# Performance work log

Hardware: AMD Instinct MI355X
Metric: run time of the kernel (lower is better)

Reference implementation:

```python
import jax, jax.numpy as jnp
import numpy as np

N_QUBITS = 4
N_LAYERS = 2
PROJ_DIM = 64
B = 262144
C64 = jnp.complex64


def setup_inputs() -> dict:
    key = jax.random.key(0)
    ks = jax.random.split(key, 4)
    x = jax.random.normal(ks[0], (B, N_QUBITS), dtype=jnp.float32)
    # TorchLayer default init: uniform(0, 2*pi)
    weights = jax.random.uniform(ks[1], (N_LAYERS, N_QUBITS, 3), dtype=jnp.float32) * (2.0 * np.pi)
    W = jax.random.normal(ks[2], (PROJ_DIM, N_QUBITS), dtype=jnp.float32) * 0.5
    b = jnp.zeros((PROJ_DIM,), dtype=jnp.float32)
    gamma = jnp.ones((PROJ_DIM,), dtype=jnp.float32)
    beta = jnp.zeros((PROJ_DIM,), dtype=jnp.float32)
    return {"x": x, "weights": weights, "W": W, "b": b, "gamma": gamma, "beta": beta}


def _apply_1q(state, U, w):
    # state: (B, 2,2,2,2); U: (2,2) shared or (B,2,2) per-sample
    s = jnp.moveaxis(state, 1 + w, -1)
    if U.ndim == 3:
        s = jnp.einsum('b...j,bij->b...i', s, U)
    else:
        s = s @ U.T
    return jnp.moveaxis(s, -1, 1 + w)


def _apply_cnot(state, c, t):
    s = jnp.moveaxis(state, (1 + c, 1 + t), (-2, -1))
    s = jnp.concatenate([s[..., :1, :], s[..., 1:, ::-1]], axis=-2)
    return jnp.moveaxis(s, (-2, -1), (1 + c, 1 + t))


def _rot_matrix(phi, theta, omega):
    # PennyLane Rot = RZ(omega) @ RY(theta) @ RZ(phi)
    c = jnp.cos(theta / 2).astype(C64)
    s = jnp.sin(theta / 2).astype(C64)
    ep = jnp.exp(-0.5j * (phi + omega).astype(C64))
    em = jnp.exp(0.5j * (phi - omega).astype(C64))
    return jnp.array(0, C64) + jnp.stack([
        jnp.stack([ep * c, -em * s]),
        jnp.stack([jnp.conj(em) * s, jnp.conj(ep) * c])], axis=0)


def _circuit(angles, weights):
    # angles: (B, n) real; returns (B, n) PauliZ expvals
    n = N_QUBITS
    Bn = angles.shape[0]
    state = jnp.zeros((Bn, 2 ** n), dtype=C64).at[:, 0].set(1.0)
    state = state.reshape((Bn,) + (2,) * n)
    # AngleEmbedding: RX(angle_w) on wire w (per-sample angles)
    half = angles / 2
    cos_h = jnp.cos(half).astype(C64)
    isin_h = (-1j) * jnp.sin(half).astype(C64)
    for w in range(n):
        U = jnp.stack([jnp.stack([cos_h[:, w], isin_h[:, w]], -1),
                       jnp.stack([isin_h[:, w], cos_h[:, w]], -1)], -2)  # (B,2,2)
        state = _apply_1q(state, U, w)
    # StronglyEntanglingLayers: Rot on each wire, then CNOT ring with range r
    for l in range(N_LAYERS):
        for w in range(n):
            U = _rot_matrix(weights[l, w, 0], weights[l, w, 1], weights[l, w, 2])
            state = _apply_1q(state, U, w)
        r = l % (n - 1) + 1
        for w in range(n):
            state = _apply_cnot(state, w, (w + r) % n)
    probs = jnp.abs(state) ** 2  # (B,2,...,2)
    sign = jnp.array([1.0, -1.0], dtype=jnp.float32)
    zs = []
    for w in range(n):
        axes = tuple(a for a in range(1, n + 1) if a != 1 + w)
        zs.append(probs.sum(axis=axes) @ sign)
    return jnp.stack(zs, -1)  # (B, n)


def reference(x, weights, W, b, gamma, beta):
    angles = jnp.tanh(x) * np.pi
    q = _circuit(angles, weights)            # (B, n_qubits)
    q = jax.nn.softmax(q, axis=-1)
    h = q @ W.T + b                          # (B, proj_dim)
    mu = h.mean(axis=-1, keepdims=True)
    var = ((h - mu) ** 2).mean(axis=-1, keepdims=True)
    hn = (h - mu) * jax.lax.rsqrt(var + 1e-5)
    return hn * gamma + beta
```

## Files before the change

### kernel.cpp

```cpp
#include <hip/hip_runtime.h>
#include <cstdint>


#define WS_VRT 0
#define WS_VIT 256
#define WS_A   512
#define WS_B0  768
#define WS_G   832
#define WS_g   848
#define WS_C0  852

__global__ __launch_bounds__(64) void qb_setup(const float* __restrict__ wts,
                                               const float* __restrict__ W,
                                               const float* __restrict__ bias,
                                               const float* __restrict__ gamma,
                                               float* __restrict__ ws) {
    const int lane = threadIdx.x;
    const int row  = lane >> 2;
    const int cg   = lane & 3;

    float ur[4], ui[4];
    #pragma unroll
    for (int c = 0; c < 4; ++c) {
        ur[c] = (row == 4*cg + c) ? 1.f : 0.f;
        ui[c] = 0.f;
    }

    #pragma unroll
    for (int l = 0; l < 2; ++l) {
        #pragma unroll
        for (int w = 0; w < 4; ++w) {
            const float ph = wts[l*12 + w*3 + 0];
            const float th = wts[l*12 + w*3 + 1];
            const float om = wts[l*12 + w*3 + 2];
            float st, ct; __sincosf(0.5f*th, &st, &ct);
            float sp, cp; __sincosf(0.5f*(ph+om), &sp, &cp);
            float sm, cm; __sincosf(0.5f*(ph-om), &sm, &cm);
            const float a00r =  cp*ct, a00i = -sp*ct;
            const float a01r = -cm*st, a01i = -sm*st;
            const float a10r =  cm*st, a10i = -sm*st;
            const float a11r =  cp*ct, a11i =  sp*ct;
            const int m8 = 8 >> w;
            const int xm = m8 << 2;
            const bool hi = (row & m8) != 0;
            #pragma unroll
            for (int c = 0; c < 4; ++c) {
                const float pr = __shfl_xor(ur[c], xm, 64);
                const float pi = __shfl_xor(ui[c], xm, 64);
                float nr, ni;
                if (!hi) {
                    nr = a00r*ur[c] - a00i*ui[c] + a01r*pr - a01i*pi;
                    ni = a00r*ui[c] + a00i*ur[c] + a01r*pi + a01i*pr;
                } else {
                    nr = a11r*ur[c] - a11i*ui[c] + a10r*pr - a10i*pi;
                    ni = a11r*ui[c] + a11i*ur[c] + a10r*pi + a10i*pr;
                }
                ur[c] = nr; ui[c] = ni;
            }
        }
        const int rr = (l == 0) ? 1 : 2;
        #pragma unroll
        for (int w = 0; w < 4; ++w) {
            const int cmk = 8 >> w;
            const int tmk = 8 >> ((w + rr) & 3);
            const int src = (row & cmk) ? (row ^ tmk) : row;
            const int srcLane = src*4 + cg;
            #pragma unroll
            for (int c = 0; c < 4; ++c) {
                ur[c] = __shfl(ur[c], srcLane, 64);
                ui[c] = __shfl(ui[c], srcLane, 64);
            }
        }
    }

    #pragma unroll
    for (int c = 0; c < 4; ++c) {
        const int col = 4*cg + c;
        const int p = __popc(col) & 3;
        float vr, vi;
        if (p == 0)      { vr =  ur[c]; vi =  ui[c]; }
        else if (p == 1) { vr =  ui[c]; vi = -ur[c]; }
        else if (p == 2) { vr = -ur[c]; vi = -ui[c]; }
        else             { vr = -ui[c]; vi =  ur[c]; }
        ws[WS_VRT + col*16 + row] = vr;
        ws[WS_VIT + col*16 + row] = vi;
    }

    {
        const int k = lane;
        float w0 = W[k*4+0], w1 = W[k*4+1], w2 = W[k*4+2], w3 = W[k*4+3];
        float bk = bias[k];
        auto wsum = [](float v) {
            #pragma unroll
            for (int o = 32; o; o >>= 1) v += __shfl_xor(v, o, 64);
            return v;
        };
        const float inv64 = 1.f/64.f;
        const float m0 = wsum(w0)*inv64, m1 = wsum(w1)*inv64;
        const float m2 = wsum(w2)*inv64, m3 = wsum(w3)*inv64;
        const float bm = wsum(bk)*inv64;
        float cc[4] = {w0-m0, w1-m1, w2-m2, w3-m3};
        const float bc = bk - bm;
        const float gk = gamma[k];
        #pragma unroll
        for (int w = 0; w < 4; ++w) ws[WS_A + k*4 + w] = cc[w]*gk;
        ws[WS_B0 + k] = bc*gk;
        #pragma unroll
        for (int a = 0; a < 4; ++a)
            #pragma unroll
            for (int b2 = a; b2 < 4; ++b2) {
                const float s = wsum(cc[a]*cc[b2])*inv64;
                if (k == 0) {
                    ws[WS_G + a*4 + b2] = s;
                    ws[WS_G + b2*4 + a] = s;
                }
            }
        #pragma unroll
        for (int a = 0; a < 4; ++a) {
            const float s = wsum(bc*cc[a])*inv64;
            if (k == 0) ws[WS_g + a] = s;
        }
        {
            const float s = wsum(bc*bc)*inv64;
            if (k == 0) ws[WS_C0] = s;
        }
    }
}

__global__ __launch_bounds__(256, 4) void qb_main(const float* __restrict__ x,
                                                  const float* __restrict__ beta,
                                                  const float* __restrict__ ws,
                                                  float* __restrict__ out) {
    __shared__ __align__(16) float4 sq[256];
    __shared__ float sinv[256];

    const int tid  = threadIdx.x;
    const int wv   = tid >> 6;
    const int lane = tid & 63;

    const int sample = blockIdx.x * 256 + tid;
    const float4 xv = ((const float4*)x)[sample];
    const int k4t = lane & 15;
    float4 A4[4];
    #pragma unroll
    for (int u = 0; u < 4; ++u) A4[u] = ((const float4*)(ws + WS_A))[k4t*4 + u];
    const float4 B04v = ((const float4*)(ws + WS_B0))[k4t];
    const float4 Bt4v = ((const float4*)beta)[k4t];

    float m[16];
    {
        const float xa[4] = {xv.x, xv.y, xv.z, xv.w};
        float c4[4], s4[4];
        #pragma unroll
        for (int w = 0; w < 4; ++w) {
            const float h = tanhf(xa[w]) * 1.5707963267948966f;
            __sincosf(h, &s4[w], &c4[w]);
        }
        const float e01[4] = {c4[0]*c4[1], c4[0]*s4[1], s4[0]*c4[1], s4[0]*s4[1]};
        const float e23[4] = {c4[2]*c4[3], c4[2]*s4[3], s4[2]*c4[3], s4[2]*s4[3]};
        #pragma unroll
        for (int j = 0; j < 16; ++j) m[j] = e01[j>>2]*e23[j&3];
    }

    float r[16], si[16];
    #pragma unroll
    for (int i = 0; i < 16; ++i) { r[i] = 0.f; si[i] = 0.f; }
    #pragma unroll
    for (int j = 0; j < 16; ++j) {
        const float mj = m[j];
        #pragma unroll
        for (int i = 0; i < 16; ++i) {
            r[i]  = fmaf(ws[WS_VRT + j*16 + i], mj, r[i]);
            si[i] = fmaf(ws[WS_VIT + j*16 + i], mj, si[i]);
        }
    }

    float z0 = 0.f, z1 = 0.f, z2 = 0.f, z3 = 0.f;
    #pragma unroll
    for (int i = 0; i < 16; ++i) {
        const float p = r[i]*r[i] + si[i]*si[i];
        z0 += (i & 8) ? -p : p;
        z1 += (i & 4) ? -p : p;
        z2 += (i & 2) ? -p : p;
        z3 += (i & 1) ? -p : p;
    }
    const float mx = fmaxf(fmaxf(z0, z1), fmaxf(z2, z3));
    const float e0 = __expf(z0-mx), e1 = __expf(z1-mx);
    const float e2 = __expf(z2-mx), e3 = __expf(z3-mx);
    const float rs = 1.f / (e0+e1+e2+e3);
    const float qx = e0*rs, qy = e1*rs, qz = e2*rs, qw = e3*rs;

    float var = ws[WS_C0];
    {
        const float qa[4] = {qx, qy, qz, qw};
        #pragma unroll
        for (int a = 0; a < 4; ++a) {
            float t = 2.f * ws[WS_g + a];
            #pragma unroll
            for (int b2 = 0; b2 < 4; ++b2) t = fmaf(ws[WS_G + a*4 + b2], qa[b2], t);
            var = fmaf(qa[a], t, var);
        }
    }
    const float inv = rsqrtf(var + 1e-5f);

    sq[wv*64 + lane]   = make_float4(qx, qy, qz, qw);
    sinv[wv*64 + lane] = inv;

    const float B04[4] = {B04v.x, B04v.y, B04v.z, B04v.w};
    const float Bt4[4] = {Bt4v.x, Bt4v.y, Bt4v.z, Bt4v.w};
    float4* outv = (float4*)out + (size_t)blockIdx.x * 4096 + wv * 1024 + lane;
    const float4* qld = sq + wv*64 + (lane >> 4);
    const float*  ild = sinv + wv*64 + (lane >> 4);
    #pragma unroll
    for (int iter = 0; iter < 16; ++iter) {
        const float4 q  = qld[iter*4];
        const float  iv = ild[iter*4];
        float4 o;
        float* op = (float*)&o;
        #pragma unroll
        for (int u = 0; u < 4; ++u) {
            float t = B04[u];
            t = fmaf(A4[u].x, q.x, t);
            t = fmaf(A4[u].y, q.y, t);
            t = fmaf(A4[u].z, q.z, t);
            t = fmaf(A4[u].w, q.w, t);
            op[u] = fmaf(t, iv, Bt4[u]);
        }
        outv[iter*64] = o;
    }
}

extern "C" void kernel_launch(void* const* d_in, const int* in_sizes, int n_in,
                              void* d_out, int out_size, void* d_ws, size_t ws_size,
                              hipStream_t stream) {
    const float* x     = (const float*)d_in[0];
    const float* wts   = (const float*)d_in[1];
    const float* W     = (const float*)d_in[2];
    const float* bias  = (const float*)d_in[3];
    const float* gamma = (const float*)d_in[4];
    const float* beta  = (const float*)d_in[5];
    float* out = (float*)d_out;
    float* ws  = (float*)d_ws;
    const int B = in_sizes[0] / 4;

    hipLaunchKernelGGL(qb_setup, dim3(1), dim3(64), 0, stream, wts, W, bias, gamma, ws);
    hipLaunchKernelGGL(qb_main, dim3(B / 256), dim3(256), 0, stream, x, beta, ws, out);
}
```

Baseline: 96.26 us.

## Split fused kernel into compute pass and output expansion pass via output scratch

The fused per-sample kernel is split in two. The first kernel runs the circuit, softmax and variance, and stores each sample's q vector and inverse std in the first five floats of that sample's own output row. A second kernel with a fixed 2048-block grid reads those values back, does the 64-wide affine expansion, and writes fully coalesced float4 output in a grid-stride pattern. The goal is to free the compute kernel from the LDS staging and occupancy limits, and to let the store-heavy expansion run at full occupancy. The cost is an extra launch, scattered small writes followed by reads of the output buffer, and reliance on each wave reading a slot before overwriting it.

```diff
diff --git a/kernel.cpp b/kernel.cpp
--- a/kernel.cpp
+++ b/kernel.cpp
@@ -127,25 +127,11 @@
     }
 }
 
-__global__ __launch_bounds__(256, 4) void qb_main(const float* __restrict__ x,
-                                                  const float* __restrict__ beta,
+__global__ __launch_bounds__(256) void qb_compute(const float* __restrict__ x,
                                                   const float* __restrict__ ws,
                                                   float* __restrict__ out) {
-    __shared__ __align__(16) float4 sq[256];
-    __shared__ float sinv[256];
-
-    const int tid  = threadIdx.x;
-    const int wv   = tid >> 6;
-    const int lane = tid & 63;
-
-    const int sample = blockIdx.x * 256 + tid;
+    const int sample = blockIdx.x * 256 + threadIdx.x;
     const float4 xv = ((const float4*)x)[sample];
-    const int k4t = lane & 15;
-    float4 A4[4];
-    #pragma unroll
-    for (int u = 0; u < 4; ++u) A4[u] = ((const float4*)(ws + WS_A))[k4t*4 + u];
-    const float4 B04v = ((const float4*)(ws + WS_B0))[k4t];
-    const float4 Bt4v = ((const float4*)beta)[k4t];
 
     float m[16];
     {
@@ -203,18 +189,41 @@
     }
     const float inv = rsqrtf(var + 1e-5f);
 
-    sq[wv*64 + lane]   = make_float4(qx, qy, qz, qw);
-    sinv[wv*64 + lane] = inv;
-
+    float* slot = out + (size_t)sample * 64;
+    *(float4*)slot = make_float4(qx, qy, qz, qw);
+    slot[4] = inv;
+}
+
+__global__ __launch_bounds__(256) void qb_expand(const float* __restrict__ beta,
+                                                 const float* __restrict__ ws,
+                                                 float* out) {
+    const int tid = threadIdx.x;
+    const int kg  = tid & 15;
+
+    float4 A4[4];
+    #pragma unroll
+    for (int u = 0; u < 4; ++u) A4[u] = ((const float4*)(ws + WS_A))[kg*4 + u];
+    const float4 B04v = ((const float4*)(ws + WS_B0))[kg];
+    const float4 Bt4v = ((const float4*)beta)[kg];
     const float B04[4] = {B04v.x, B04v.y, B04v.z, B04v.w};
     const float Bt4[4] = {Bt4v.x, Bt4v.y, Bt4v.z, Bt4v.w};
-    float4* outv = (float4*)out + (size_t)blockIdx.x * 4096 + wv * 1024 + lane;
-    const float4* qld = sq + wv*64 + (lane >> 4);
-    const float*  ild = sinv + wv*64 + (lane >> 4);
-    #pragma unroll
-    for (int iter = 0; iter < 16; ++iter) {
-        const float4 q  = qld[iter*4];
-        const float  iv = ild[iter*4];
+
+    const size_t f0 = (size_t)blockIdx.x * 256 + tid;
+    const size_t stride = (size_t)2048 * 256;
+
+    float4 qs[8]; float ivs[8];
+    #pragma unroll
+    for (int it = 0; it < 8; ++it) {
+        const size_t f = f0 + (size_t)it * stride;
+        const float* slot = out + (f >> 4) * 64;
+        qs[it]  = *(const float4*)slot;
+        ivs[it] = slot[4];
+    }
+    #pragma unroll
+    for (int it = 0; it < 8; ++it) {
+        const size_t f = f0 + (size_t)it * stride;
+        const float4 q  = qs[it];
+        const float  iv = ivs[it];
         float4 o;
         float* op = (float*)&o;
         #pragma unroll
@@ -226,7 +235,7 @@
             t = fmaf(A4[u].w, q.w, t);
             op[u] = fmaf(t, iv, Bt4[u]);
         }
-        outv[iter*64] = o;
+        ((float4*)out)[f] = o;
     }
 }
 
@@ -243,6 +252,7 @@
     float* ws  = (float*)d_ws;
     const int B = in_sizes[0] / 4;
 
-    hipLaunchKernelGGL(qb_setup, dim3(1), dim3(64), 0, stream, wts, W, bias, gamma, ws);
-    hipLaunchKernelGGL(qb_main, dim3(B / 256), dim3(256), 0, stream, x, beta, ws, out);
-}
+    hipLaunchKernelGGL(qb_setup,   dim3(1),       dim3(64),  0, stream, wts, W, bias, gamma, ws);
+    hipLaunchKernelGGL(qb_compute, dim3(B / 256), dim3(256), 0, stream, x, ws, out);
+    hipLaunchKernelGGL(qb_expand,  dim3(2048),    dim3(256), 0, stream, beta, ws, out);
+}
```

Measured after the change: 108.0 us. 12.1% more time.

## Use constant address space loads and per-thread row output instead of LDS transpose

Applied to the files above, without the earlier changes.

Casts the workspace and beta pointers to the constant address space so that uniform matrix and projection loads can become scalar loads. A row-major copy of the unitary is added so each output amplitude is reduced in turn, which lowers register pressure. The LDS-staged, coalesced output write is dropped: each thread now writes its own 256-byte row with strided float4 stores, and the block size falls from 256 to 128. The risk is that per-thread strided stores coalesce worse than the previous wave-contiguous stores, and this is a store-bound kernel.

```diff
diff --git a/kernel.cpp b/kernel.cpp
--- a/kernel.cpp
+++ b/kernel.cpp
@@ -1,6 +1,12 @@
 #include <hip/hip_runtime.h>
 #include <cstdint>
 
+
+#define CONST_AS __attribute__((address_space(4)))
+template <typename T>
+__device__ inline const CONST_AS T* as_const4(const T* p) {
+    return (const CONST_AS T*)(uintptr_t)p;
+}
 
 #define WS_VRT 0
 #define WS_VIT 256
@@ -9,6 +15,8 @@
 #define WS_G   832
 #define WS_g   848
 #define WS_C0  852
+#define WS_VR2 864
+#define WS_VI2 1120
 
 __global__ __launch_bounds__(64) void qb_setup(const float* __restrict__ wts,
                                                const float* __restrict__ W,
@@ -84,6 +92,8 @@
         else             { vr = -ui[c]; vi =  ur[c]; }
         ws[WS_VRT + col*16 + row] = vr;
         ws[WS_VIT + col*16 + row] = vi;
+        ws[WS_VR2 + row*16 + col] = vr;
+        ws[WS_VI2 + row*16 + col] = vi;
     }
 
     {
@@ -127,25 +137,14 @@
     }
 }
 
-__global__ __launch_bounds__(256, 4) void qb_main(const float* __restrict__ x,
-                                                  const float* __restrict__ beta,
-                                                  const float* __restrict__ ws,
-                                                  float* __restrict__ out) {
-    __shared__ __align__(16) float4 sq[256];
-    __shared__ float sinv[256];
-
-    const int tid  = threadIdx.x;
-    const int wv   = tid >> 6;
-    const int lane = tid & 63;
-
-    const int sample = blockIdx.x * 256 + tid;
+__global__ __launch_bounds__(128) void qb_main(const float* __restrict__ x,
+                                               const float* __restrict__ beta,
+                                               const float* __restrict__ ws,
+                                               float* __restrict__ out) {
+    const int sample = blockIdx.x * 128 + threadIdx.x;
     const float4 xv = ((const float4*)x)[sample];
-    const int k4t = lane & 15;
-    float4 A4[4];
-    #pragma unroll
-    for (int u = 0; u < 4; ++u) A4[u] = ((const float4*)(ws + WS_A))[k4t*4 + u];
-    const float4 B04v = ((const float4*)(ws + WS_B0))[k4t];
-    const float4 Bt4v = ((const float4*)beta)[k4t];
+    const CONST_AS float* V = as_const4(ws);
+    const CONST_AS float* Bt = as_const4(beta);
 
     float m[16];
     {
@@ -162,71 +161,57 @@
         for (int j = 0; j < 16; ++j) m[j] = e01[j>>2]*e23[j&3];
     }
 
-    float r[16], si[16];
-    #pragma unroll
-    for (int i = 0; i < 16; ++i) { r[i] = 0.f; si[i] = 0.f; }
-    #pragma unroll
-    for (int j = 0; j < 16; ++j) {
-        const float mj = m[j];
-        #pragma unroll
-        for (int i = 0; i < 16; ++i) {
-            r[i]  = fmaf(ws[WS_VRT + j*16 + i], mj, r[i]);
-            si[i] = fmaf(ws[WS_VIT + j*16 + i], mj, si[i]);
-        }
-    }
-
     float z0 = 0.f, z1 = 0.f, z2 = 0.f, z3 = 0.f;
     #pragma unroll
     for (int i = 0; i < 16; ++i) {
-        const float p = r[i]*r[i] + si[i]*si[i];
+        float ri = 0.f, ti = 0.f;
+        #pragma unroll
+        for (int j = 0; j < 16; ++j) {
+            ri = fmaf(V[WS_VR2 + i*16 + j], m[j], ri);
+            ti = fmaf(V[WS_VI2 + i*16 + j], m[j], ti);
+        }
+        const float p = ri*ri + ti*ti;
         z0 += (i & 8) ? -p : p;
         z1 += (i & 4) ? -p : p;
         z2 += (i & 2) ? -p : p;
         z3 += (i & 1) ? -p : p;
     }
+
     const float mx = fmaxf(fmaxf(z0, z1), fmaxf(z2, z3));
     const float e0 = __expf(z0-mx), e1 = __expf(z1-mx);
     const float e2 = __expf(z2-mx), e3 = __expf(z3-mx);
     const float rs = 1.f / (e0+e1+e2+e3);
     const float qx = e0*rs, qy = e1*rs, qz = e2*rs, qw = e3*rs;
 
-    float var = ws[WS_C0];
+    float var = V[WS_C0];
     {
         const float qa[4] = {qx, qy, qz, qw};
         #pragma unroll
         for (int a = 0; a < 4; ++a) {
-            float t = 2.f * ws[WS_g + a];
-            #pragma unroll
-            for (int b2 = 0; b2 < 4; ++b2) t = fmaf(ws[WS_G + a*4 + b2], qa[b2], t);
+            float t = 2.f * V[WS_g + a];
+            #pragma unroll
+            for (int b2 = 0; b2 < 4; ++b2) t = fmaf(V[WS_G + a*4 + b2], qa[b2], t);
             var = fmaf(qa[a], t, var);
         }
     }
     const float inv = rsqrtf(var + 1e-5f);
 
-    sq[wv*64 + lane]   = make_float4(qx, qy, qz, qw);
-    sinv[wv*64 + lane] = inv;
-
-    const float B04[4] = {B04v.x, B04v.y, B04v.z, B04v.w};
-    const float Bt4[4] = {Bt4v.x, Bt4v.y, Bt4v.z, Bt4v.w};
-    float4* outv = (float4*)out + (size_t)blockIdx.x * 4096 + wv * 1024 + lane;
-    const float4* qld = sq + wv*64 + (lane >> 4);
-    const float*  ild = sinv + wv*64 + (lane >> 4);
-    #pragma unroll
-    for (int iter = 0; iter < 16; ++iter) {
-        const float4 q  = qld[iter*4];
-        const float  iv = ild[iter*4];
+    float* slot = out + (size_t)sample * 64;
+    #pragma unroll
+    for (int kb = 0; kb < 16; ++kb) {
         float4 o;
         float* op = (float*)&o;
         #pragma unroll
         for (int u = 0; u < 4; ++u) {
-            float t = B04[u];
-            t = fmaf(A4[u].x, q.x, t);
-            t = fmaf(A4[u].y, q.y, t);
-            t = fmaf(A4[u].z, q.z, t);
-            t = fmaf(A4[u].w, q.w, t);
-            op[u] = fmaf(t, iv, Bt4[u]);
-        }
-        outv[iter*64] = o;
+            const int k = kb*4 + u;
+            float t = V[WS_B0 + k];
+            t = fmaf(V[WS_A + k*4 + 0], qx, t);
+            t = fmaf(V[WS_A + k*4 + 1], qy, t);
+            t = fmaf(V[WS_A + k*4 + 2], qz, t);
+            t = fmaf(V[WS_A + k*4 + 3], qw, t);
+            op[u] = fmaf(t, inv, Bt[k]);
+        }
+        *(float4*)(slot + kb*4) = o;
     }
 }
 
@@ -243,6 +228,6 @@
     float* ws  = (float*)d_ws;
     const int B = in_sizes[0] / 4;
 
-    hipLaunchKernelGGL(qb_setup, dim3(1), dim3(64), 0, stream, wts, W, bias, gamma, ws);
-    hipLaunchKernelGGL(qb_main, dim3(B / 256), dim3(256), 0, stream, x, beta, ws, out);
-}
+    hipLaunchKernelGGL(qb_setup, dim3(1),       dim3(64),  0, stream, wts, W, bias, gamma, ws);
+    hipLaunchKernelGGL(qb_main,  dim3(B / 128), dim3(128), 0, stream, x, beta, ws, out);
+}
```

After: 110.8 us. 15.1% more time.
